# Optimization experiments

Hardware: AMD Instinct MI355X
Metric: run time of the kernel (lower is better)

## Reference

```python
import jax, jax.numpy as jnp
import numpy as np

K = 8192      # num_embeddings
D = 256       # patch_hw = H*W
BETA = 0.25
DECAY = 0.99
EPS = 1e-5


def setup_inputs() -> dict:
    key = jax.random.key(0)
    k1, k2, k3 = jax.random.split(key, 3)
    z = jax.random.normal(k1, (32, 512, 16, 16), dtype=jnp.float32)
    embedding = jax.random.normal(k2, (K, D), dtype=jnp.float32)
    ema_cluster_size = jnp.zeros((K,), dtype=jnp.float32)
    ema_embed_sum = jax.random.normal(k3, (K, D), dtype=jnp.float32)
    return {"z": z, "embedding": embedding,
            "ema_cluster_size": ema_cluster_size,
            "ema_embed_sum": ema_embed_sum}


def reference(z, embedding, ema_cluster_size, ema_embed_sum):
    B, C, H, W = z.shape
    flat = z.reshape(B * C, H * W)                       # (N, D)
    dist = (jnp.sum(flat * flat, axis=1, keepdims=True)
            - 2.0 * flat @ embedding.T
            + jnp.sum(embedding * embedding, axis=1))
    indices = jnp.argmin(dist, axis=1)                   # (N,)
    quantized = embedding[indices].reshape(B, C, H, W)

    # EMA codebook update (training mode); stats are detached
    flat_sg = jax.lax.stop_gradient(flat)
    n_i = jax.ops.segment_sum(jnp.ones_like(flat_sg[:, 0]), indices,
                              num_segments=K)            # (K,)
    e_i = jax.ops.segment_sum(flat_sg, indices, num_segments=K)  # (K, D)
    new_ecs = ema_cluster_size * DECAY + (1.0 - DECAY) * n_i
    new_ees = ema_embed_sum * DECAY + (1.0 - DECAY) * e_i
    n_tot = jnp.sum(new_ecs)
    smoothed = (new_ecs + EPS) / (n_tot + K * EPS) * n_tot
    new_embedding = new_ees / smoothed[:, None]

    commit_loss = jnp.mean((jax.lax.stop_gradient(quantized) - z) ** 2)
    q_st = z + jax.lax.stop_gradient(quantized - z)      # straight-through
    return (q_st, BETA * commit_loss, indices.reshape(B, C),
            new_embedding, new_ecs, new_ees)
```

## Files before the change

### kernel.cpp

```cpp
#include <hip/hip_runtime.h>
#include <hip/hip_bf16.h>

#define NROWS 16384
#define DDIM  256
#define KEMB  8192
#define DECAYF 0.99f
#define ONE_MINUS_DECAY 0.01f
#define EPSF 1e-5f

#define O_QST   0
#define O_LOSS  4194304
#define O_IDX   4194305
#define O_EMB   4210689
#define O_ECS   6307841
#define O_EES   6316033

typedef __attribute__((ext_vector_type(8))) short short8;
typedef __attribute__((ext_vector_type(4))) float f32x4;

static __device__ __forceinline__ unsigned short f2bf(float x) {
    unsigned int u = __float_as_uint(x);
    return (unsigned short)((u + 0x7fffu + ((u >> 16) & 1u)) >> 16);
}
static __device__ __forceinline__ float bf2f(unsigned short h) {
    return __uint_as_float(((unsigned int)h) << 16);
}

static __device__ __forceinline__ void gload16(const unsigned short* g, unsigned short* l) {
    __builtin_amdgcn_global_load_lds(
        (const __attribute__((address_space(1))) unsigned int*)g,
        (__attribute__((address_space(3))) unsigned int*)l, 16, 0, 0);
}

__global__ __launch_bounds__(256) void prep_all(const float* __restrict__ z,
                                                const float* __restrict__ emb,
                                                const float* __restrict__ ecs_in,
                                                const float* __restrict__ ees_in,
                                                float* __restrict__ enorm,
                                                unsigned short* __restrict__ eh,
                                                unsigned short* __restrict__ el,
                                                unsigned short* __restrict__ zh,
                                                unsigned short* __restrict__ zl,
                                                float* __restrict__ o_ecs,
                                                float* __restrict__ o_ees,
                                                float* __restrict__ part_e,
                                                unsigned long long* __restrict__ key64) {
    const int b = blockIdx.x;
    const int w = threadIdx.x >> 6;
    const int lane = threadIdx.x & 63;
    if (b < 2048) {
        const int k = b * 4 + w;
        const int base = k * DDIM + lane * 4;
        const float4 v = *(const float4*)&emb[base];
        ushort4 h, l;
        {
            const float* vp = (const float*)&v;
            unsigned short hh;
            hh = f2bf(vp[0]); h.x = hh; l.x = f2bf(vp[0] - bf2f(hh));
            hh = f2bf(vp[1]); h.y = hh; l.y = f2bf(vp[1] - bf2f(hh));
            hh = f2bf(vp[2]); h.z = hh; l.z = f2bf(vp[2] - bf2f(hh));
            hh = f2bf(vp[3]); h.w = hh; l.w = f2bf(vp[3] - bf2f(hh));
        }
        *(ushort4*)&eh[base] = h;
        *(ushort4*)&el[base] = l;
        const float4 s = *(const float4*)&ees_in[base];
        float4 so;
        so.x = DECAYF * s.x; so.y = DECAYF * s.y; so.z = DECAYF * s.z; so.w = DECAYF * s.w;
        *(float4*)&o_ees[base] = so;
        float sum = v.x * v.x + v.y * v.y + v.z * v.z + v.w * v.w;
        for (int o = 32; o; o >>= 1) sum += __shfl_down(sum, o);
        __shared__ float sc[4];
        if (lane == 0) {
            enorm[k] = sum;
            const float c = DECAYF * ecs_in[k];
            o_ecs[k] = c;
            sc[w] = c;
        }
        __syncthreads();
        if (threadIdx.x == 0) part_e[b] = sc[0] + sc[1] + sc[2] + sc[3];
    } else {
        const int n = (b - 2048) * 4 + w;
        const int base = n * DDIM + lane * 4;
        const float4 v = *(const float4*)&z[base];
        ushort4 h, l;
        {
            const float* vp = (const float*)&v;
            unsigned short hh;
            hh = f2bf(vp[0]); h.x = hh; l.x = f2bf(vp[0] - bf2f(hh));
            hh = f2bf(vp[1]); h.y = hh; l.y = f2bf(vp[1] - bf2f(hh));
            hh = f2bf(vp[2]); h.z = hh; l.z = f2bf(vp[2] - bf2f(hh));
            hh = f2bf(vp[3]); h.w = hh; l.w = f2bf(vp[3] - bf2f(hh));
        }
        *(ushort4*)&zh[base] = h;
        *(ushort4*)&zl[base] = l;
        if (lane == 0) key64[n] = ~0ull;
    }
}

__global__ __launch_bounds__(512) void argmin_mfma(const unsigned short* __restrict__ zh,
                                                   const unsigned short* __restrict__ zl,
                                                   const unsigned short* __restrict__ eh,
                                                   const unsigned short* __restrict__ el,
                                                   const float* __restrict__ enorm,
                                                   unsigned long long* __restrict__ key64) {
    __shared__ unsigned short Ah[2][256][32];
    __shared__ unsigned short Al[2][256][32];
    __shared__ unsigned short Bh[2][256][32];
    __shared__ unsigned short Bl[2][256][32];

    const int tid = threadIdx.x;
    const int lane = tid & 63;
    const int wid = tid >> 6;
    const int wm = wid >> 2;
    const int wn = wid & 3;
    const int tx = lane & 15, quad = lane >> 4;

    const int row0 = blockIdx.x * 256;
    const int col0 = blockIdx.y * 256;

    const int r16 = lane >> 2;
    const int gc8 = (((lane & 3) ^ ((lane >> 3) & 3)) * 8);
    const int sw = (quad ^ ((tx >> 1) & 3)) * 8;

    const unsigned short* gsrc = (wid < 2) ? zh : (wid < 4) ? zl : (wid < 6) ? eh : el;
    unsigned short* lds0 = (wid < 2) ? &Ah[0][0][0] : (wid < 4) ? &Al[0][0][0]
                         : (wid < 6) ? &Bh[0][0][0] : &Bl[0][0][0];
    const int gbase0 = (wid < 4) ? row0 : col0;
    const int slab0 = (wid & 1) * 8;

    auto stage = [&](int b, int dk) {
#pragma unroll
        for (int i = 0; i < 8; i++) {
            const int lr = (slab0 + i) * 16;
            gload16(&gsrc[(size_t)(gbase0 + lr + r16) * DDIM + dk + gc8],
                    lds0 + b * 8192 + lr * 32);
        }
    };

    f32x4 acc[8][4];
#pragma unroll
    for (int i = 0; i < 8; i++)
#pragma unroll
        for (int j = 0; j < 4; j++) acc[i][j] = (f32x4){0.f, 0.f, 0.f, 0.f};

    stage(0, 0);
    __syncthreads();

    for (int d8 = 0; d8 < 8; d8++) {
        const int cur = d8 & 1;
        if (d8 < 7) stage(cur ^ 1, (d8 + 1) * 32);

        short8 bH[4], bL[4];
        const int bbase = wn * 64 + tx;
#pragma unroll
        for (int nj = 0; nj < 4; nj++) {
            bH[nj] = *(const short8*)&Bh[cur][bbase + nj * 16][sw];
            bL[nj] = *(const short8*)&Bl[cur][bbase + nj * 16][sw];
        }
        const int abase = wm * 128 + tx;
#pragma unroll
        for (int mi = 0; mi < 8; mi++) {
            const short8 aH = *(const short8*)&Ah[cur][abase + mi * 16][sw];
            const short8 aL = *(const short8*)&Al[cur][abase + mi * 16][sw];
#pragma unroll
            for (int nj = 0; nj < 4; nj++) {
                acc[mi][nj] = __builtin_amdgcn_mfma_f32_16x16x32_bf16(aH, bH[nj], acc[mi][nj], 0, 0, 0);
                acc[mi][nj] = __builtin_amdgcn_mfma_f32_16x16x32_bf16(aL, bH[nj], acc[mi][nj], 0, 0, 0);
                acc[mi][nj] = __builtin_amdgcn_mfma_f32_16x16x32_bf16(aH, bL[nj], acc[mi][nj], 0, 0, 0);
            }
        }
        __syncthreads();
    }

    float en[4];
    int colv[4];
#pragma unroll
    for (int nj = 0; nj < 4; nj++) {
        colv[nj] = col0 + wn * 64 + nj * 16 + tx;
        en[nj] = enorm[colv[nj]];
    }
#pragma unroll
    for (int mi = 0; mi < 8; mi++) {
#pragma unroll
        for (int r = 0; r < 4; r++) {
            unsigned long long best = ~0ull;
#pragma unroll
            for (int nj = 0; nj < 4; nj++) {
                float d = en[nj] - 2.0f * acc[mi][nj][r];
                unsigned int db = __float_as_uint(d);
                db = (db & 0x80000000u) ? ~db : (db | 0x80000000u);
                unsigned long long key = ((unsigned long long)db << 32) | (unsigned int)colv[nj];
                if (key < best) best = key;
            }
#pragma unroll
            for (int m = 1; m < 16; m <<= 1) {
                unsigned long long o = __shfl_xor(best, m);
                if (o < best) best = o;
            }
            if (tx == 0)
                atomicMin(&key64[row0 + wm * 128 + mi * 16 + quad * 4 + r], best);
        }
    }
}

__global__ __launch_bounds__(256) void quant_stats(const float* __restrict__ z,
                                                   const float* __restrict__ emb,
                                                   const unsigned long long* __restrict__ key64,
                                                   float* __restrict__ o_qst,
                                                   float* __restrict__ o_idx,
                                                   float* __restrict__ o_ecs,
                                                   float* __restrict__ o_ees,
                                                   float* __restrict__ part_q) {
    const int w = threadIdx.x >> 6;
    const int lane = threadIdx.x & 63;
    const int nbase = blockIdx.x * 16 + w * 4;
    const int d0 = lane * 4;
    float ploc = 0.f;
#pragma unroll
    for (int r = 0; r < 4; r++) {
        const int n = nbase + r;
        const int k = (int)(key64[n] & 0xFFFFFFFFull);
        const float4 zv = *(const float4*)&z[n * DDIM + d0];
        const float4 ev = *(const float4*)&emb[k * DDIM + d0];
        const float dx = ev.x - zv.x, dy = ev.y - zv.y, dz2 = ev.z - zv.z, dw = ev.w - zv.w;
        float4 q;
        q.x = zv.x + dx; q.y = zv.y + dy; q.z = zv.z + dz2; q.w = zv.w + dw;
        *(float4*)&o_qst[n * DDIM + d0] = q;
        ploc += dx * dx + dy * dy + dz2 * dz2 + dw * dw;
        if (lane == 0) {
            o_idx[n] = (float)k;
            atomicAdd(&o_ecs[k], ONE_MINUS_DECAY);
        }
        atomicAdd(&o_ees[k * DDIM + d0 + 0], ONE_MINUS_DECAY * zv.x);
        atomicAdd(&o_ees[k * DDIM + d0 + 1], ONE_MINUS_DECAY * zv.y);
        atomicAdd(&o_ees[k * DDIM + d0 + 2], ONE_MINUS_DECAY * zv.z);
        atomicAdd(&o_ees[k * DDIM + d0 + 3], ONE_MINUS_DECAY * zv.w);
    }
    for (int o = 32; o; o >>= 1) ploc += __shfl_down(ploc, o);
    __shared__ float sh[4];
    if (lane == 0) sh[w] = ploc;
    __syncthreads();
    if (threadIdx.x == 0) part_q[blockIdx.x] = sh[0] + sh[1] + sh[2] + sh[3];
}

__global__ __launch_bounds__(256) void finalize_kernel(const float* __restrict__ o_ecs,
                                                       const float* __restrict__ o_ees,
                                                       const float* __restrict__ part_e,
                                                       const float* __restrict__ part_q,
                                                       float* __restrict__ o_emb,
                                                       float* __restrict__ o_loss) {
    const int k = blockIdx.x;
    const int d = threadIdx.x;
    __shared__ float red[256];
    float s = 0.f;
    for (int i = d; i < 2048; i += 256) s += part_e[i];
    red[d] = s;
    __syncthreads();
    for (int o = 128; o; o >>= 1) {
        if (d < o) red[d] += red[d + o];
        __syncthreads();
    }
    const float ntot = red[0] + ONE_MINUS_DECAY * (float)NROWS;
    const float ecs = o_ecs[k];
    const float sm = (ecs + EPSF) / (ntot + (float)KEMB * EPSF) * ntot;
    o_emb[k * DDIM + d] = o_ees[k * DDIM + d] / sm;
    if (k == 0) {
        __syncthreads();
        float s2 = 0.f;
        for (int i = d; i < 1024; i += 256) s2 += part_q[i];
        red[d] = s2;
        __syncthreads();
        for (int o = 128; o; o >>= 1) {
            if (d < o) red[d] += red[d + o];
            __syncthreads();
        }
        if (d == 0) o_loss[0] = 0.25f * red[0] / (float)(NROWS * DDIM);
    }
}

extern "C" void kernel_launch(void* const* d_in, const int* in_sizes, int n_in,
                              void* d_out, int out_size, void* d_ws, size_t ws_size,
                              hipStream_t stream) {
    const float* z   = (const float*)d_in[0];
    const float* emb = (const float*)d_in[1];
    const float* ecs = (const float*)d_in[2];
    const float* ees = (const float*)d_in[3];

    float* out = (float*)d_out;
    char*  ws  = (char*)d_ws;

    float* enorm = (float*)ws;
    unsigned long long* key64 = (unsigned long long*)(ws + 32768);
    float* part_e = (float*)(ws + 163840);
    float* part_q = part_e + 2048;

    const size_t big0 = 163840 + 8192 + 4096;
    const size_t bigbytes = (size_t)(NROWS + KEMB) * DDIM * 2 * 2;
    unsigned short *zh, *zl, *ehp, *elp;
    if (ws_size >= big0 + bigbytes) {
        zh  = (unsigned short*)(ws + big0);
        zl  = zh + NROWS * DDIM;
        ehp = zl + NROWS * DDIM;
        elp = ehp + KEMB * DDIM;
    } else {
        zh  = (unsigned short*)(out + O_QST);
        zl  = zh + NROWS * DDIM;
        ehp = (unsigned short*)(out + O_EMB);
        elp = ehp + KEMB * DDIM;
    }

    prep_all<<<6144, 256, 0, stream>>>(z, emb, ecs, ees, enorm, ehp, elp,
                                       zh, zl, out + O_ECS, out + O_EES,
                                       part_e, key64);
    argmin_mfma<<<dim3(NROWS / 256, KEMB / 256), 512, 0, stream>>>(zh, zl, ehp, elp, enorm, key64);
    quant_stats<<<NROWS / 16, 256, 0, stream>>>(z, emb, key64, out + O_QST, out + O_IDX,
                                                out + O_ECS, out + O_EES, part_q);
    finalize_kernel<<<KEMB, DDIM, 0, stream>>>(out + O_ECS, out + O_EES,
                                               part_e, part_q,
                                               out + O_EMB, out + O_LOSS);
}
```

Before: 389.7 us.

## Restructure distance GEMM main loop into phased ping-pong schedule with setprio

Splits each K-step of the split-bf16 MFMA distance GEMM into four phases of two M-subtiles each. Every phase loads its LDS fragments, waits on a barrier, and runs its MFMA cluster under raised wave priority. Global prefetch of the next buffer is issued after the B fragments load, and vmcnt is waited only at the end of the step. The goal is to overlap LDS reads and global staging with matrix-core work across waves, in the style of HipKittens/CK ping-pong scheduling. The cost is many more s_barrier calls per iteration, which could serialize waves if the phases are unbalanced.

```diff
diff --git a/kernel.cpp b/kernel.cpp
--- a/kernel.cpp
+++ b/kernel.cpp
@@ -144,32 +144,52 @@
         for (int j = 0; j < 4; j++) acc[i][j] = (f32x4){0.f, 0.f, 0.f, 0.f};
 
     stage(0, 0);
-    __syncthreads();
-
-    for (int d8 = 0; d8 < 8; d8++) {
-        const int cur = d8 & 1;
-        if (d8 < 7) stage(cur ^ 1, (d8 + 1) * 32);
-
-        short8 bH[4], bL[4];
-        const int bbase = wn * 64 + tx;
-#pragma unroll
-        for (int nj = 0; nj < 4; nj++) {
-            bH[nj] = *(const short8*)&Bh[cur][bbase + nj * 16][sw];
-            bL[nj] = *(const short8*)&Bl[cur][bbase + nj * 16][sw];
-        }
-        const int abase = wm * 128 + tx;
-#pragma unroll
-        for (int mi = 0; mi < 8; mi++) {
-            const short8 aH = *(const short8*)&Ah[cur][abase + mi * 16][sw];
-            const short8 aL = *(const short8*)&Al[cur][abase + mi * 16][sw];
+    asm volatile("s_waitcnt vmcnt(0)" ::: "memory");
+    __builtin_amdgcn_s_barrier();
+
+    short8 bH[4], bL[4];
+    const int abase = wm * 128 + tx;
+    const int bbase = wn * 64 + tx;
+
+    for (int t = 0; t < 8; ++t) {
+        const int cur = t & 1;
+#pragma unroll
+        for (int ph = 0; ph < 4; ++ph) {
+            const int mi0 = ph * 2, mi1 = ph * 2 + 1;
+            const short8 aH0 = *(const short8*)&Ah[cur][abase + mi0 * 16][sw];
+            const short8 aL0 = *(const short8*)&Al[cur][abase + mi0 * 16][sw];
+            const short8 aH1 = *(const short8*)&Ah[cur][abase + mi1 * 16][sw];
+            const short8 aL1 = *(const short8*)&Al[cur][abase + mi1 * 16][sw];
+            if (ph == 0) {
+#pragma unroll
+                for (int nj = 0; nj < 4; nj++) {
+                    bH[nj] = *(const short8*)&Bh[cur][bbase + nj * 16][sw];
+                    bL[nj] = *(const short8*)&Bl[cur][bbase + nj * 16][sw];
+                }
+                if (t < 7) stage(cur ^ 1, (t + 1) * 32);
+            }
+            __builtin_amdgcn_s_barrier();
+            asm volatile("s_waitcnt lgkmcnt(0)" ::: "memory");
+            __builtin_amdgcn_sched_barrier(0);
+            __builtin_amdgcn_s_setprio(1);
 #pragma unroll
             for (int nj = 0; nj < 4; nj++) {
-                acc[mi][nj] = __builtin_amdgcn_mfma_f32_16x16x32_bf16(aH, bH[nj], acc[mi][nj], 0, 0, 0);
-                acc[mi][nj] = __builtin_amdgcn_mfma_f32_16x16x32_bf16(aL, bH[nj], acc[mi][nj], 0, 0, 0);
-                acc[mi][nj] = __builtin_amdgcn_mfma_f32_16x16x32_bf16(aH, bL[nj], acc[mi][nj], 0, 0, 0);
-            }
-        }
-        __syncthreads();
+                acc[mi0][nj] = __builtin_amdgcn_mfma_f32_16x16x32_bf16(aH0, bH[nj], acc[mi0][nj], 0, 0, 0);
+                acc[mi0][nj] = __builtin_amdgcn_mfma_f32_16x16x32_bf16(aL0, bH[nj], acc[mi0][nj], 0, 0, 0);
+                acc[mi0][nj] = __builtin_amdgcn_mfma_f32_16x16x32_bf16(aH0, bL[nj], acc[mi0][nj], 0, 0, 0);
+            }
+#pragma unroll
+            for (int nj = 0; nj < 4; nj++) {
+                acc[mi1][nj] = __builtin_amdgcn_mfma_f32_16x16x32_bf16(aH1, bH[nj], acc[mi1][nj], 0, 0, 0);
+                acc[mi1][nj] = __builtin_amdgcn_mfma_f32_16x16x32_bf16(aL1, bH[nj], acc[mi1][nj], 0, 0, 0);
+                acc[mi1][nj] = __builtin_amdgcn_mfma_f32_16x16x32_bf16(aH1, bL[nj], acc[mi1][nj], 0, 0, 0);
+            }
+            __builtin_amdgcn_s_setprio(0);
+            if (ph == 3) {
+                asm volatile("s_waitcnt vmcnt(0)" ::: "memory");
+            }
+            __builtin_amdgcn_s_barrier();
+        }
     }
 
     float en[4];
```

Result: slower. 414.4 us (+6.3%).

## Replace float atomic scatter of EMA sums with per-code bucket lists and gather

Applied to the files above, without the earlier changes.

The per-element float atomicAdd scatter into the EMA embed sums is replaced by per-code index buckets (capacity 64, plus an overflow list). The finalize kernel then gathers the assigned z rows per code and computes the new sums, counts and embedding in one pass, so the read-modify-write of the ees tensor in prep is also dropped. This removes a large volume of contended global atomics, at the cost of serial gather loops in finalize and a slow overflow scan if some codes are assigned very often.

```diff
diff --git a/kernel.cpp b/kernel.cpp
--- a/kernel.cpp
+++ b/kernel.cpp
@@ -7,6 +7,7 @@
 #define DECAYF 0.99f
 #define ONE_MINUS_DECAY 0.01f
 #define EPSF 1e-5f
+#define CAP  64
 
 #define O_QST   0
 #define O_LOSS  4194304
@@ -35,15 +36,14 @@
 __global__ __launch_bounds__(256) void prep_all(const float* __restrict__ z,
                                                 const float* __restrict__ emb,
                                                 const float* __restrict__ ecs_in,
-                                                const float* __restrict__ ees_in,
                                                 float* __restrict__ enorm,
                                                 unsigned short* __restrict__ eh,
                                                 unsigned short* __restrict__ el,
                                                 unsigned short* __restrict__ zh,
                                                 unsigned short* __restrict__ zl,
-                                                float* __restrict__ o_ecs,
-                                                float* __restrict__ o_ees,
                                                 float* __restrict__ part_e,
+                                                unsigned int* __restrict__ cnt,
+                                                unsigned int* __restrict__ ovf_cnt,
                                                 unsigned long long* __restrict__ key64) {
     const int b = blockIdx.x;
     const int w = threadIdx.x >> 6;
@@ -63,21 +63,19 @@
         }
         *(ushort4*)&eh[base] = h;
         *(ushort4*)&el[base] = l;
-        const float4 s = *(const float4*)&ees_in[base];
-        float4 so;
-        so.x = DECAYF * s.x; so.y = DECAYF * s.y; so.z = DECAYF * s.z; so.w = DECAYF * s.w;
-        *(float4*)&o_ees[base] = so;
         float sum = v.x * v.x + v.y * v.y + v.z * v.z + v.w * v.w;
         for (int o = 32; o; o >>= 1) sum += __shfl_down(sum, o);
         __shared__ float sc[4];
         if (lane == 0) {
             enorm[k] = sum;
-            const float c = DECAYF * ecs_in[k];
-            o_ecs[k] = c;
-            sc[w] = c;
-        }
-        __syncthreads();
-        if (threadIdx.x == 0) part_e[b] = sc[0] + sc[1] + sc[2] + sc[3];
+            sc[w] = DECAYF * ecs_in[k];
+            cnt[k] = 0u;
+        }
+        __syncthreads();
+        if (threadIdx.x == 0) {
+            part_e[b] = sc[0] + sc[1] + sc[2] + sc[3];
+            if (b == 0) ovf_cnt[0] = 0u;
+        }
     } else {
         const int n = (b - 2048) * 4 + w;
         const int base = n * DDIM + lane * 4;
@@ -208,8 +206,10 @@
                                                    const unsigned long long* __restrict__ key64,
                                                    float* __restrict__ o_qst,
                                                    float* __restrict__ o_idx,
-                                                   float* __restrict__ o_ecs,
-                                                   float* __restrict__ o_ees,
+                                                   unsigned int* __restrict__ cnt,
+                                                   unsigned short* __restrict__ bucket,
+                                                   unsigned int* __restrict__ ovf_cnt,
+                                                   unsigned int* __restrict__ ovf,
                                                    float* __restrict__ part_q) {
     const int w = threadIdx.x >> 6;
     const int lane = threadIdx.x & 63;
@@ -229,12 +229,14 @@
         ploc += dx * dx + dy * dy + dz2 * dz2 + dw * dw;
         if (lane == 0) {
             o_idx[n] = (float)k;
-            atomicAdd(&o_ecs[k], ONE_MINUS_DECAY);
-        }
-        atomicAdd(&o_ees[k * DDIM + d0 + 0], ONE_MINUS_DECAY * zv.x);
-        atomicAdd(&o_ees[k * DDIM + d0 + 1], ONE_MINUS_DECAY * zv.y);
-        atomicAdd(&o_ees[k * DDIM + d0 + 2], ONE_MINUS_DECAY * zv.z);
-        atomicAdd(&o_ees[k * DDIM + d0 + 3], ONE_MINUS_DECAY * zv.w);
+            const unsigned int pos = atomicAdd(&cnt[k], 1u);
+            if (pos < CAP) {
+                bucket[(size_t)k * CAP + pos] = (unsigned short)n;
+            } else {
+                const unsigned int oi = atomicAdd(ovf_cnt, 1u);
+                ovf[oi] = ((unsigned int)k << 16) | (unsigned int)n;
+            }
+        }
     }
     for (int o = 32; o; o >>= 1) ploc += __shfl_down(ploc, o);
     __shared__ float sh[4];
@@ -243,10 +245,17 @@
     if (threadIdx.x == 0) part_q[blockIdx.x] = sh[0] + sh[1] + sh[2] + sh[3];
 }
 
-__global__ __launch_bounds__(256) void finalize_kernel(const float* __restrict__ o_ecs,
-                                                       const float* __restrict__ o_ees,
+__global__ __launch_bounds__(256) void finalize_kernel(const float* __restrict__ z,
+                                                       const float* __restrict__ ecs_in,
+                                                       const float* __restrict__ ees_in,
+                                                       const unsigned int* __restrict__ cnt,
+                                                       const unsigned short* __restrict__ bucket,
+                                                       const unsigned int* __restrict__ ovf_cnt,
+                                                       const unsigned int* __restrict__ ovf,
                                                        const float* __restrict__ part_e,
                                                        const float* __restrict__ part_q,
+                                                       float* __restrict__ o_ecs,
+                                                       float* __restrict__ o_ees,
                                                        float* __restrict__ o_emb,
                                                        float* __restrict__ o_loss) {
     const int k = blockIdx.x;
@@ -261,9 +270,28 @@
         __syncthreads();
     }
     const float ntot = red[0] + ONE_MINUS_DECAY * (float)NROWS;
-    const float ecs = o_ecs[k];
-    const float sm = (ecs + EPSF) / (ntot + (float)KEMB * EPSF) * ntot;
-    o_emb[k * DDIM + d] = o_ees[k * DDIM + d] / sm;
+
+    const unsigned int c = cnt[k];
+    const int cb = (int)(c < CAP ? c : CAP);
+    float ei = 0.f;
+    for (int i = 0; i < cb; i++) {
+        const int n = (int)bucket[(size_t)k * CAP + i];
+        ei += z[(size_t)n * DDIM + d];
+    }
+    const unsigned int on = ovf_cnt[0];
+    if (on) {
+        for (unsigned int i = 0; i < on; i++) {
+            const unsigned int e = ovf[i];
+            if ((int)(e >> 16) == k) ei += z[(size_t)(e & 0xFFFFu) * DDIM + d];
+        }
+    }
+    const float new_ees = DECAYF * ees_in[(size_t)k * DDIM + d] + ONE_MINUS_DECAY * ei;
+    const float new_ecs = DECAYF * ecs_in[k] + ONE_MINUS_DECAY * (float)c;
+    const float sm = (new_ecs + EPSF) / (ntot + (float)KEMB * EPSF) * ntot;
+    o_ees[(size_t)k * DDIM + d] = new_ees;
+    o_emb[(size_t)k * DDIM + d] = new_ees / sm;
+    if (d == 0) o_ecs[k] = new_ecs;
+
     if (k == 0) {
         __syncthreads();
         float s2 = 0.f;
@@ -293,8 +321,12 @@
     unsigned long long* key64 = (unsigned long long*)(ws + 32768);
     float* part_e = (float*)(ws + 163840);
     float* part_q = part_e + 2048;
-
-    const size_t big0 = 163840 + 8192 + 4096;
+    unsigned int* cnt = (unsigned int*)(ws + 176128);
+    unsigned int* ovf_cnt = (unsigned int*)(ws + 208896);
+    unsigned int* ovf = (unsigned int*)(ws + 209152);
+    unsigned short* bucket = (unsigned short*)(ws + 274688);
+
+    const size_t big0 = 274688 + (size_t)KEMB * CAP * 2;
     const size_t bigbytes = (size_t)(NROWS + KEMB) * DDIM * 2 * 2;
     unsigned short *zh, *zl, *ehp, *elp;
     if (ws_size >= big0 + bigbytes) {
@@ -309,13 +341,13 @@
         elp = ehp + KEMB * DDIM;
     }
 
-    prep_all<<<6144, 256, 0, stream>>>(z, emb, ecs, ees, enorm, ehp, elp,
-                                       zh, zl, out + O_ECS, out + O_EES,
-                                       part_e, key64);
+    prep_all<<<6144, 256, 0, stream>>>(z, emb, ecs, enorm, ehp, elp,
+                                       zh, zl, part_e, cnt, ovf_cnt, key64);
     argmin_mfma<<<dim3(NROWS / 256, KEMB / 256), 512, 0, stream>>>(zh, zl, ehp, elp, enorm, key64);
     quant_stats<<<NROWS / 16, 256, 0, stream>>>(z, emb, key64, out + O_QST, out + O_IDX,
-                                                out + O_ECS, out + O_EES, part_q);
-    finalize_kernel<<<KEMB, DDIM, 0, stream>>>(out + O_ECS, out + O_EES,
+                                                cnt, bucket, ovf_cnt, ovf, part_q);
+    finalize_kernel<<<KEMB, DDIM, 0, stream>>>(z, ecs, ees, cnt, bucket, ovf_cnt, ovf,
                                                part_e, part_q,
+                                               out + O_ECS, out + O_EES,
                                                out + O_EMB, out + O_LOSS);
 }
```

New measurement: 749.7 us. +92.4%, slower.
